# Optimization experiments

Measured on AMD Instinct MI355X. Metric: run time of the kernel, lower is better.

Reference implementation:

```python
import jax, jax.numpy as jnp
import numpy as np

TOP_K = 2


def setup_inputs() -> dict:
    key = jax.random.key(0)
    ks = jax.random.split(key, 5)
    B, S, D, F, E = 2, 1024, 2048, 4096, 8
    scale_in = 1.0 / np.sqrt(D)
    scale_f = 1.0 / np.sqrt(F)
    return {
        "hidden_states": jax.random.normal(ks[0], (B, S, D), dtype=jnp.float32),
        "gate_w": jax.random.normal(ks[1], (D, E), dtype=jnp.float32) * scale_in,
        "w1": jax.random.normal(ks[2], (E, D, F), dtype=jnp.float32) * scale_in,
        "w3": jax.random.normal(ks[3], (E, D, F), dtype=jnp.float32) * scale_in,
        "w2": jax.random.normal(ks[4], (E, F, D), dtype=jnp.float32) * scale_f,
    }


def reference(hidden_states, gate_w, w1, w3, w2):
    orig_shape = hidden_states.shape
    D = orig_shape[-1]
    x = hidden_states.reshape(-1, D)                      # [T, D]
    E = gate_w.shape[-1]

    # Router: replicated linear (no bias), logits in fp32.
    router_logits = (x @ gate_w).astype(jnp.float32)      # [T, E]
    probs = jax.nn.softmax(router_logits, axis=-1)        # [T, E]
    topk_vals, topk_idx = jax.lax.top_k(probs, TOP_K)     # [T, K]
    # renormalize=False: use raw softmax probs of the selected experts.
    # Scatter top-k weights back to a dense [T, E] combine matrix.
    onehot = jax.nn.one_hot(topk_idx, E, dtype=probs.dtype)        # [T, K, E]
    combine = jnp.einsum("tke,tk->te", onehot, topk_vals)          # [T, E]

    # Dense-over-experts SwiGLU (reference for the fused grouped-GEMM).
    gate = jax.nn.silu(jnp.einsum("td,edf->etf", x, w1))  # [E, T, F]
    up = jnp.einsum("td,edf->etf", x, w3)                 # [E, T, F]
    expert_out = jnp.einsum("etf,efd->etd", gate * up, w2)  # [E, T, D]

    # Combine (this is the TP all-reduce + weighted sum in vllm).
    y = jnp.einsum("te,etd->td", combine, expert_out)     # [T, D]
    return y.reshape(orig_shape)
```

## Files before the change

kernel.cpp:

```cpp
#include <hip/hip_runtime.h>

typedef short v8s __attribute__((ext_vector_type(8)));
typedef float v4f __attribute__((ext_vector_type(4)));

#define T_TOK 2048
#define DD 2048
#define FF 4096
#define EE 8
#define BM 128
#define BN 128
#define BK 64
#define MT_MAX 40
#define MAXROWS 5120

#define WS_COUNTS 0
#define WS_FILL   32
#define WS_ROWOFF 64
#define WS_TOPE   128
#define WS_TOPW   (WS_TOPE + T_TOK * 2 * 4)
#define WS_IDS    (WS_TOPW + T_TOK * 2 * 4)
#define WS_WTS    (WS_IDS + MAXROWS * 4)
#define WS_ZERO   (WS_WTS + MAXROWS * 4)
#define WS_H      73984ul

#define SWZ(r, kb) ((r) * 128 + ((kb) ^ ((((r) ^ ((r) >> 3)) & 7) << 4)))

static __device__ __forceinline__ short f2bf(float f) {
  return __builtin_bit_cast(short, static_cast<__bf16>(f));
}

__global__ __launch_bounds__(256) void router_k(
    const float* __restrict__ x, const float* __restrict__ gw,
    int* __restrict__ counts, int* __restrict__ tope, float* __restrict__ topw) {
  const int lane = threadIdx.x & 63;
  const int t = blockIdx.x * 4 + (threadIdx.x >> 6);
  if (t >= T_TOK) return;
  float acc[EE] = {0.f, 0.f, 0.f, 0.f, 0.f, 0.f, 0.f, 0.f};
  const float* xr = x + (size_t)t * DD;
  for (int i = 0; i < DD / 64; ++i) {
    int k = i * 64 + lane;
    float xv = xr[k];
    const v4f* g = (const v4f*)(gw + (size_t)k * EE);
    v4f g0 = g[0], g1 = g[1];
    acc[0] += xv * g0[0]; acc[1] += xv * g0[1]; acc[2] += xv * g0[2]; acc[3] += xv * g0[3];
    acc[4] += xv * g1[0]; acc[5] += xv * g1[1]; acc[6] += xv * g1[2]; acc[7] += xv * g1[3];
  }
  #pragma unroll
  for (int e = 0; e < EE; ++e) {
    #pragma unroll
    for (int off = 32; off > 0; off >>= 1) acc[e] += __shfl_xor(acc[e], off);
  }
  if (lane == 0) {
    float m = acc[0];
    #pragma unroll
    for (int e = 1; e < EE; ++e) m = fmaxf(m, acc[e]);
    float p[EE], s = 0.f;
    #pragma unroll
    for (int e = 0; e < EE; ++e) { p[e] = expf(acc[e] - m); s += p[e]; }
    float inv = 1.f / s;
    #pragma unroll
    for (int e = 0; e < EE; ++e) p[e] *= inv;
    int e1 = 0;
    #pragma unroll
    for (int e = 1; e < EE; ++e) if (p[e] > p[e1]) e1 = e;
    int e2 = (e1 == 0) ? 1 : 0;
    #pragma unroll
    for (int e = 0; e < EE; ++e) if (e != e1 && p[e] > p[e2]) e2 = e;
    tope[2 * t] = e1;  tope[2 * t + 1] = e2;
    topw[2 * t] = p[e1]; topw[2 * t + 1] = p[e2];
    atomicAdd(&counts[e1], 1);
    atomicAdd(&counts[e2], 1);
  }
}

__global__ void offsets_k(const int* __restrict__ counts, int* __restrict__ rowoff) {
  if (threadIdx.x == 0) {
    int off = 0;
    #pragma unroll
    for (int e = 0; e < EE; ++e) {
      rowoff[e] = off;
      off += ((counts[e] + BM - 1) / BM) * BM;
    }
  }
}

__global__ __launch_bounds__(256) void scatter_k(
    const int* __restrict__ tope, const float* __restrict__ topw,
    const int* __restrict__ rowoff, int* __restrict__ fill,
    int* __restrict__ ids, float* __restrict__ wts) {
  const int t = blockIdx.x * 256 + threadIdx.x;
  if (t >= T_TOK) return;
  #pragma unroll
  for (int j = 0; j < 2; ++j) {
    int e = tope[2 * t + j];
    int pos = rowoff[e] + atomicAdd(&fill[e], 1);
    ids[pos] = t;
    wts[pos] = topw[2 * t + j];
  }
}

__global__ __launch_bounds__(256, 2) void gemm1_k(
    const float* __restrict__ x, const float* __restrict__ w1,
    const float* __restrict__ w3, const int* __restrict__ counts,
    const int* __restrict__ rowoff, const int* __restrict__ ids,
    unsigned short* __restrict__ H) {
  const int nt = blockIdx.x, mt = blockIdx.y;
  int expert = -1;
  #pragma unroll
  for (int e = 0; e < EE; ++e) {
    int rs = rowoff[e];
    int tl = (counts[e] + BM - 1) / BM;
    if (mt * BM >= rs && mt * BM < rs + tl * BM) expert = e;
  }
  if (expert < 0) return;
  const int m0 = mt * BM, n0 = nt * BN;

  __shared__ unsigned short sA[BM * BK];
  __shared__ unsigned short sB0[BN * BK];
  __shared__ unsigned short sB1[BN * BK];

  const int tid = threadIdx.x;
  const int lane = tid & 63;
  const int wid = tid >> 6;
  const int wm = (wid >> 1) * 64, wn = (wid & 1) * 64;
  const int lr = lane & 15, lg = lane >> 4;

  const int a_row0 = tid >> 3;
  const int a_kc = (tid & 7) * 8;
  const float* aptr[4];
  #pragma unroll
  for (int g = 0; g < 4; ++g)
    aptr[g] = x + (size_t)ids[m0 + a_row0 + g * 32] * DD + a_kc;

  const int b_f4 = (tid & 31) * 4;
  const int b_k8 = (tid >> 5) * 8;
  const float* wb1 = w1 + (size_t)expert * DD * FF + n0 + b_f4 + (size_t)b_k8 * FF;
  const float* wb3 = w3 + (size_t)expert * DD * FF + n0 + b_f4 + (size_t)b_k8 * FF;

  v4f acc1[4][4], acc3[4][4];
  #pragma unroll
  for (int i = 0; i < 4; ++i)
    #pragma unroll
    for (int j = 0; j < 4; ++j) {
      acc1[i][j] = (v4f){0.f, 0.f, 0.f, 0.f};
      acc3[i][j] = (v4f){0.f, 0.f, 0.f, 0.f};
    }

  for (int kt = 0; kt < DD / BK; ++kt) {
    #pragma unroll
    for (int g = 0; g < 4; ++g) {
      const float* p = aptr[g] + (size_t)kt * BK;
      v4f u0 = *(const v4f*)p;
      v4f u1 = *(const v4f*)(p + 4);
      v8s h;
      h[0] = f2bf(u0[0]); h[1] = f2bf(u0[1]); h[2] = f2bf(u0[2]); h[3] = f2bf(u0[3]);
      h[4] = f2bf(u1[0]); h[5] = f2bf(u1[1]); h[6] = f2bf(u1[2]); h[7] = f2bf(u1[3]);
      *(v8s*)((char*)sA + SWZ(a_row0 + g * 32, a_kc * 2)) = h;
    }
    {
      const float* p = wb1 + (size_t)kt * BK * FF;
      v4f r[8];
      #pragma unroll
      for (int j = 0; j < 8; ++j) r[j] = *(const v4f*)(p + (size_t)j * FF);
      #pragma unroll
      for (int c = 0; c < 4; ++c) {
        v8s h;
        #pragma unroll
        for (int j = 0; j < 8; ++j) h[j] = f2bf(r[j][c]);
        *(v8s*)((char*)sB0 + SWZ(b_f4 + c, b_k8 * 2)) = h;
      }
      p = wb3 + (size_t)kt * BK * FF;
      #pragma unroll
      for (int j = 0; j < 8; ++j) r[j] = *(const v4f*)(p + (size_t)j * FF);
      #pragma unroll
      for (int c = 0; c < 4; ++c) {
        v8s h;
        #pragma unroll
        for (int j = 0; j < 8; ++j) h[j] = f2bf(r[j][c]);
        *(v8s*)((char*)sB1 + SWZ(b_f4 + c, b_k8 * 2)) = h;
      }
    }
    __syncthreads();
    #pragma unroll
    for (int ks = 0; ks < 2; ++ks) {
      const int kb = ks * 64 + lg * 16;
      v8s a[4], b1[4], b3[4];
      #pragma unroll
      for (int m = 0; m < 4; ++m)
        a[m] = *(const v8s*)((const char*)sA + SWZ(wm + m * 16 + lr, kb));
      #pragma unroll
      for (int n = 0; n < 4; ++n) {
        b1[n] = *(const v8s*)((const char*)sB0 + SWZ(wn + n * 16 + lr, kb));
        b3[n] = *(const v8s*)((const char*)sB1 + SWZ(wn + n * 16 + lr, kb));
      }
      #pragma unroll
      for (int m = 0; m < 4; ++m)
        #pragma unroll
        for (int n = 0; n < 4; ++n) {
          acc1[m][n] = __builtin_amdgcn_mfma_f32_16x16x32_bf16(a[m], b1[n], acc1[m][n], 0, 0, 0);
          acc3[m][n] = __builtin_amdgcn_mfma_f32_16x16x32_bf16(a[m], b3[n], acc3[m][n], 0, 0, 0);
        }
    }
    __syncthreads();
  }
  #pragma unroll
  for (int m = 0; m < 4; ++m)
    #pragma unroll
    for (int n = 0; n < 4; ++n)
      #pragma unroll
      for (int r = 0; r < 4; ++r) {
        int row = wm + m * 16 + lg * 4 + r;
        int col = wn + n * 16 + lr;
        float g = acc1[m][n][r];
        float u = acc3[m][n][r];
        float hv = (g / (1.f + expf(-g))) * u;
        H[(size_t)(m0 + row) * FF + (n0 + col)] = (unsigned short)f2bf(hv);
      }
}

__global__ __launch_bounds__(256, 2) void gemm2_k(
    const unsigned short* __restrict__ H, const float* __restrict__ w2,
    const int* __restrict__ counts, const int* __restrict__ rowoff,
    const int* __restrict__ ids, const float* __restrict__ wts,
    float* __restrict__ out) {
  const int nt = blockIdx.x, mt = blockIdx.y;
  int expert = -1;
  #pragma unroll
  for (int e = 0; e < EE; ++e) {
    int rs = rowoff[e];
    int tl = (counts[e] + BM - 1) / BM;
    if (mt * BM >= rs && mt * BM < rs + tl * BM) expert = e;
  }
  if (expert < 0) return;
  const int m0 = mt * BM, n0 = nt * BN;

  __shared__ unsigned short sA[BM * BK];
  __shared__ unsigned short sB[BN * BK];

  const int tid = threadIdx.x;
  const int lane = tid & 63;
  const int wid = tid >> 6;
  const int wm = (wid >> 1) * 64, wn = (wid & 1) * 64;
  const int lr = lane & 15, lg = lane >> 4;

  const int a_row0 = tid >> 3;
  const int a_kc = (tid & 7) * 8;
  const unsigned short* ha = H + (size_t)(m0 + a_row0) * FF + a_kc;
  const int b_f4 = (tid & 31) * 4;
  const int b_k8 = (tid >> 5) * 8;
  const float* wb = w2 + (size_t)expert * FF * DD + n0 + b_f4 + (size_t)b_k8 * DD;

  v4f acc[4][4];
  #pragma unroll
  for (int i = 0; i < 4; ++i)
    #pragma unroll
    for (int j = 0; j < 4; ++j) acc[i][j] = (v4f){0.f, 0.f, 0.f, 0.f};

  for (int kt = 0; kt < FF / BK; ++kt) {
    #pragma unroll
    for (int g = 0; g < 4; ++g) {
      v8s h = *(const v8s*)(ha + (size_t)g * 32 * FF + kt * BK);
      *(v8s*)((char*)sA + SWZ(a_row0 + g * 32, a_kc * 2)) = h;
    }
    {
      const float* p = wb + (size_t)kt * BK * DD;
      v4f r[8];
      #pragma unroll
      for (int j = 0; j < 8; ++j) r[j] = *(const v4f*)(p + (size_t)j * DD);
      #pragma unroll
      for (int c = 0; c < 4; ++c) {
        v8s h;
        #pragma unroll
        for (int j = 0; j < 8; ++j) h[j] = f2bf(r[j][c]);
        *(v8s*)((char*)sB + SWZ(b_f4 + c, b_k8 * 2)) = h;
      }
    }
    __syncthreads();
    #pragma unroll
    for (int ks = 0; ks < 2; ++ks) {
      const int kb = ks * 64 + lg * 16;
      v8s a[4], b[4];
      #pragma unroll
      for (int m = 0; m < 4; ++m)
        a[m] = *(const v8s*)((const char*)sA + SWZ(wm + m * 16 + lr, kb));
      #pragma unroll
      for (int n = 0; n < 4; ++n)
        b[n] = *(const v8s*)((const char*)sB + SWZ(wn + n * 16 + lr, kb));
      #pragma unroll
      for (int m = 0; m < 4; ++m)
        #pragma unroll
        for (int n = 0; n < 4; ++n)
          acc[m][n] = __builtin_amdgcn_mfma_f32_16x16x32_bf16(a[m], b[n], acc[m][n], 0, 0, 0);
    }
    __syncthreads();
  }
  #pragma unroll
  for (int m = 0; m < 4; ++m)
    #pragma unroll
    for (int r = 0; r < 4; ++r) {
      int row = m0 + wm + m * 16 + lg * 4 + r;
      float wgt = wts[row];
      if (wgt != 0.f) {
        float* orow = out + (size_t)ids[row] * DD + n0 + wn + lr;
        #pragma unroll
        for (int n = 0; n < 4; ++n)
          atomicAdd(orow + n * 16, wgt * acc[m][n][r]);
      }
    }
}

extern "C" void kernel_launch(void* const* d_in, const int* in_sizes, int n_in,
                              void* d_out, int out_size, void* d_ws, size_t ws_size,
                              hipStream_t stream) {
  const float* x  = (const float*)d_in[0];
  const float* gw = (const float*)d_in[1];
  const float* w1 = (const float*)d_in[2];
  const float* w3 = (const float*)d_in[3];
  const float* w2 = (const float*)d_in[4];
  float* out = (float*)d_out;
  char* ws = (char*)d_ws;

  int*   counts = (int*)(ws + WS_COUNTS);
  int*   fill   = (int*)(ws + WS_FILL);
  int*   rowoff = (int*)(ws + WS_ROWOFF);
  int*   tope   = (int*)(ws + WS_TOPE);
  float* topw   = (float*)(ws + WS_TOPW);
  int*   ids    = (int*)(ws + WS_IDS);
  float* wts    = (float*)(ws + WS_WTS);
  unsigned short* H = (unsigned short*)(ws + WS_H);

  hipMemsetAsync(ws, 0, WS_ZERO, stream);
  hipMemsetAsync(d_out, 0, (size_t)out_size * sizeof(float), stream);

  router_k<<<T_TOK / 4, 256, 0, stream>>>(x, gw, counts, tope, topw);
  offsets_k<<<1, 64, 0, stream>>>(counts, rowoff);
  scatter_k<<<T_TOK / 256, 256, 0, stream>>>(tope, topw, rowoff, fill, ids, wts);
  gemm1_k<<<dim3(FF / BN, MT_MAX), 256, 0, stream>>>(x, w1, w3, counts, rowoff, ids, H);
  gemm2_k<<<dim3(DD / BN, MT_MAX), 256, 0, stream>>>(H, w2, counts, rowoff, ids, wts, out);
}
```

Measured before the change: 550.3 us.

## Load activation tiles via direct global-to-LDS loads with XCD-aware block remapping

Replaces the register-staged A-tile loads in both grouped GEMMs with global_load_lds 16-byte transfers straight into shared memory. Gemm1 now keeps the fp32 x tile in LDS, which doubles that buffer, and converts it to bf16 when reading fragments. The swizzle is applied on the global side so the reads stay conflict-free. Block indices are also remapped so that consecutive blocks on the same XCD share weight tiles for L2 reuse, and the expert lookup is factored into a helper. The larger fp32 LDS buffer in gemm1 may cut occupancy, and the bf16 conversion is now repeated per fragment read.

Measured after the change: 659.2 us. 1.2x slower.

```diff
diff --git a/kernel.cpp b/kernel.cpp
--- a/kernel.cpp
+++ b/kernel.cpp
@@ -27,6 +27,12 @@
 
 static __device__ __forceinline__ short f2bf(float f) {
   return __builtin_bit_cast(short, static_cast<__bf16>(f));
+}
+
+static __device__ __forceinline__ void gload_lds16(const void* g, void* l) {
+  __builtin_amdgcn_global_load_lds(
+      (const __attribute__((address_space(1))) unsigned int*)g,
+      (__attribute__((address_space(3))) unsigned int*)l, 16, 0, 0);
 }
 
 __global__ __launch_bounds__(256) void router_k(
@@ -99,23 +105,40 @@
   }
 }
 
+static __device__ __forceinline__ int find_expert(
+    const int* counts, const int* rowoff, int mt) {
+  int expert = -1;
+  #pragma unroll
+  for (int e = 0; e < EE; ++e) {
+    int rs = rowoff[e];
+    int tl = (counts[e] + BM - 1) / BM;
+    if (mt * BM >= rs && mt * BM < rs + tl * BM) expert = e;
+  }
+  return expert;
+}
+
+static __device__ __forceinline__ void xcd_map(int* nt, int* mt) {
+  int gx = gridDim.x, gy = gridDim.y;
+  int nwg = gx * gy;
+  int lin = blockIdx.y * gx + blockIdx.x;
+  int q = nwg >> 3;
+  int s = (lin & 7) * q + (lin >> 3);
+  *nt = s / gy;
+  *mt = s % gy;
+}
+
 __global__ __launch_bounds__(256, 2) void gemm1_k(
     const float* __restrict__ x, const float* __restrict__ w1,
     const float* __restrict__ w3, const int* __restrict__ counts,
     const int* __restrict__ rowoff, const int* __restrict__ ids,
     unsigned short* __restrict__ H) {
-  const int nt = blockIdx.x, mt = blockIdx.y;
-  int expert = -1;
-  #pragma unroll
-  for (int e = 0; e < EE; ++e) {
-    int rs = rowoff[e];
-    int tl = (counts[e] + BM - 1) / BM;
-    if (mt * BM >= rs && mt * BM < rs + tl * BM) expert = e;
-  }
+  int nt, mt;
+  xcd_map(&nt, &mt);
+  const int expert = find_expert(counts, rowoff, mt);
   if (expert < 0) return;
   const int m0 = mt * BM, n0 = nt * BN;
 
-  __shared__ unsigned short sA[BM * BK];
+  __shared__ float sA[BM * BK];
   __shared__ unsigned short sB0[BN * BK];
   __shared__ unsigned short sB1[BN * BK];
 
@@ -125,12 +148,16 @@
   const int wm = (wid >> 1) * 64, wn = (wid & 1) * 64;
   const int lr = lane & 15, lg = lane >> 4;
 
-  const int a_row0 = tid >> 3;
-  const int a_kc = (tid & 7) * 8;
-  const float* aptr[4];
-  #pragma unroll
-  for (int g = 0; g < 4; ++g)
-    aptr[g] = x + (size_t)ids[m0 + a_row0 + g * 32] * DD + a_kc;
+  const int awr0 = wid * 32;
+  const int alrow = lane >> 4;
+  const int achk = lane & 15;
+  const float* abp[8];
+  #pragma unroll
+  for (int i = 0; i < 8; ++i) {
+    int lrow_full = i * 4 + alrow;
+    int sg = lrow_full & 7;
+    abp[i] = x + (size_t)ids[m0 + awr0 + lrow_full] * DD + ((achk ^ sg) << 2);
+  }
 
   const int b_f4 = (tid & 31) * 4;
   const int b_k8 = (tid >> 5) * 8;
@@ -148,58 +175,51 @@
 
   for (int kt = 0; kt < DD / BK; ++kt) {
     #pragma unroll
-    for (int g = 0; g < 4; ++g) {
-      const float* p = aptr[g] + (size_t)kt * BK;
-      v4f u0 = *(const v4f*)p;
-      v4f u1 = *(const v4f*)(p + 4);
-      v8s h;
-      h[0] = f2bf(u0[0]); h[1] = f2bf(u0[1]); h[2] = f2bf(u0[2]); h[3] = f2bf(u0[3]);
-      h[4] = f2bf(u1[0]); h[5] = f2bf(u1[1]); h[6] = f2bf(u1[2]); h[7] = f2bf(u1[3]);
-      *(v8s*)((char*)sA + SWZ(a_row0 + g * 32, a_kc * 2)) = h;
-    }
+    for (int i = 0; i < 8; ++i)
+      gload_lds16(abp[i] + (size_t)kt * BK, (char*)sA + (awr0 + i * 4) * 256);
     {
-      const float* p = wb1 + (size_t)kt * BK * FF;
-      v4f r[8];
-      #pragma unroll
-      for (int j = 0; j < 8; ++j) r[j] = *(const v4f*)(p + (size_t)j * FF);
+      const float* p1 = wb1 + (size_t)kt * BK * FF;
+      const float* p3 = wb3 + (size_t)kt * BK * FF;
+      v4f r1[8], r3[8];
+      #pragma unroll
+      for (int j = 0; j < 8; ++j) r1[j] = *(const v4f*)(p1 + (size_t)j * FF);
+      #pragma unroll
+      for (int j = 0; j < 8; ++j) r3[j] = *(const v4f*)(p3 + (size_t)j * FF);
       #pragma unroll
       for (int c = 0; c < 4; ++c) {
-        v8s h;
-        #pragma unroll
-        for (int j = 0; j < 8; ++j) h[j] = f2bf(r[j][c]);
-        *(v8s*)((char*)sB0 + SWZ(b_f4 + c, b_k8 * 2)) = h;
-      }
-      p = wb3 + (size_t)kt * BK * FF;
-      #pragma unroll
-      for (int j = 0; j < 8; ++j) r[j] = *(const v4f*)(p + (size_t)j * FF);
-      #pragma unroll
-      for (int c = 0; c < 4; ++c) {
-        v8s h;
-        #pragma unroll
-        for (int j = 0; j < 8; ++j) h[j] = f2bf(r[j][c]);
-        *(v8s*)((char*)sB1 + SWZ(b_f4 + c, b_k8 * 2)) = h;
+        v8s h1, h3;
+        #pragma unroll
+        for (int j = 0; j < 8; ++j) { h1[j] = f2bf(r1[j][c]); h3[j] = f2bf(r3[j][c]); }
+        *(v8s*)((char*)sB0 + SWZ(b_f4 + c, b_k8 * 2)) = h1;
+        *(v8s*)((char*)sB1 + SWZ(b_f4 + c, b_k8 * 2)) = h3;
       }
     }
     __syncthreads();
     #pragma unroll
     for (int ks = 0; ks < 2; ++ks) {
       const int kb = ks * 64 + lg * 16;
-      v8s a[4], b1[4], b3[4];
-      #pragma unroll
-      for (int m = 0; m < 4; ++m)
-        a[m] = *(const v8s*)((const char*)sA + SWZ(wm + m * 16 + lr, kb));
+      v8s b1[4], b3[4];
       #pragma unroll
       for (int n = 0; n < 4; ++n) {
         b1[n] = *(const v8s*)((const char*)sB0 + SWZ(wn + n * 16 + lr, kb));
         b3[n] = *(const v8s*)((const char*)sB1 + SWZ(wn + n * 16 + lr, kb));
       }
       #pragma unroll
-      for (int m = 0; m < 4; ++m)
+      for (int m = 0; m < 4; ++m) {
+        const int row = wm + m * 16 + lr;
+        const int sg = row & 7;
+        const int g0 = ks * 8 + lg * 2;
+        v4f c0 = *(const v4f*)((const char*)sA + row * 256 + ((g0 ^ sg) << 4));
+        v4f c1 = *(const v4f*)((const char*)sA + row * 256 + (((g0 + 1) ^ sg) << 4));
+        v8s av;
+        av[0] = f2bf(c0[0]); av[1] = f2bf(c0[1]); av[2] = f2bf(c0[2]); av[3] = f2bf(c0[3]);
+        av[4] = f2bf(c1[0]); av[5] = f2bf(c1[1]); av[6] = f2bf(c1[2]); av[7] = f2bf(c1[3]);
         #pragma unroll
         for (int n = 0; n < 4; ++n) {
-          acc1[m][n] = __builtin_amdgcn_mfma_f32_16x16x32_bf16(a[m], b1[n], acc1[m][n], 0, 0, 0);
-          acc3[m][n] = __builtin_amdgcn_mfma_f32_16x16x32_bf16(a[m], b3[n], acc3[m][n], 0, 0, 0);
+          acc1[m][n] = __builtin_amdgcn_mfma_f32_16x16x32_bf16(av, b1[n], acc1[m][n], 0, 0, 0);
+          acc3[m][n] = __builtin_amdgcn_mfma_f32_16x16x32_bf16(av, b3[n], acc3[m][n], 0, 0, 0);
         }
+      }
     }
     __syncthreads();
   }
@@ -223,14 +243,9 @@
     const int* __restrict__ counts, const int* __restrict__ rowoff,
     const int* __restrict__ ids, const float* __restrict__ wts,
     float* __restrict__ out) {
-  const int nt = blockIdx.x, mt = blockIdx.y;
-  int expert = -1;
-  #pragma unroll
-  for (int e = 0; e < EE; ++e) {
-    int rs = rowoff[e];
-    int tl = (counts[e] + BM - 1) / BM;
-    if (mt * BM >= rs && mt * BM < rs + tl * BM) expert = e;
-  }
+  int nt, mt;
+  xcd_map(&nt, &mt);
+  const int expert = find_expert(counts, rowoff, mt);
   if (expert < 0) return;
   const int m0 = mt * BM, n0 = nt * BN;
 
@@ -243,9 +258,17 @@
   const int wm = (wid >> 1) * 64, wn = (wid & 1) * 64;
   const int lr = lane & 15, lg = lane >> 4;
 
-  const int a_row0 = tid >> 3;
-  const int a_kc = (tid & 7) * 8;
-  const unsigned short* ha = H + (size_t)(m0 + a_row0) * FF + a_kc;
+  const int awr0 = wid * 32;
+  const int alrow = lane >> 3;
+  const int achk = lane & 7;
+  const unsigned short* abp[4];
+  #pragma unroll
+  for (int i = 0; i < 4; ++i) {
+    int lrow_full = i * 8 + alrow;
+    int sg = lrow_full & 7;
+    abp[i] = H + (size_t)(m0 + awr0 + lrow_full) * FF + ((achk ^ sg) << 3);
+  }
+
   const int b_f4 = (tid & 31) * 4;
   const int b_k8 = (tid >> 5) * 8;
   const float* wb = w2 + (size_t)expert * FF * DD + n0 + b_f4 + (size_t)b_k8 * DD;
@@ -258,10 +281,8 @@
 
   for (int kt = 0; kt < FF / BK; ++kt) {
     #pragma unroll
-    for (int g = 0; g < 4; ++g) {
-      v8s h = *(const v8s*)(ha + (size_t)g * 32 * FF + kt * BK);
-      *(v8s*)((char*)sA + SWZ(a_row0 + g * 32, a_kc * 2)) = h;
-    }
+    for (int i = 0; i < 4; ++i)
+      gload_lds16(abp[i] + (size_t)kt * BK, (char*)sA + (awr0 + i * 8) * 128);
     {
       const float* p = wb + (size_t)kt * BK * DD;
       v4f r[8];
@@ -281,8 +302,11 @@
       const int kb = ks * 64 + lg * 16;
       v8s a[4], b[4];
       #pragma unroll
-      for (int m = 0; m < 4; ++m)
-        a[m] = *(const v8s*)((const char*)sA + SWZ(wm + m * 16 + lr, kb));
+      for (int m = 0; m < 4; ++m) {
+        const int row = wm + m * 16 + lr;
+        const int g = ks * 4 + lg;
+        a[m] = *(const v8s*)((const char*)sA + row * 128 + ((g ^ (row & 7)) << 4));
+      }
       #pragma unroll
       for (int n = 0; n < 4; ++n)
         b[n] = *(const v8s*)((const char*)sB + SWZ(wn + n * 16 + lr, kb));
```
